# Kernel optimization log

Hardware: AMD Instinct MI355X
Metric: run time of the kernel (lower is better)

## Reference

```python
import jax, jax.numpy as jnp
import numpy as np

N, K, C, NUM_RBF, H, T = 8192, 32, 16, 16, 64, 5  # nodes, knn, channels, rbf, radial hidden, num interactions


def _levi_civita():
    e = np.zeros((3, 3, 3), np.float32)
    for i, j, k in [(0, 1, 2), (1, 2, 0), (2, 0, 1)]:
        e[i, j, k] = 1.0
        e[j, i, k] = -1.0
    return jnp.asarray(e)


def setup_inputs() -> dict:
    key = jax.random.key(0)
    ks = jax.random.split(key, 16)
    inp = {}
    inp['f0'] = jax.random.normal(ks[0], (N, C, 1), jnp.float32)
    inp['f1'] = jax.random.normal(ks[1], (N, C, 3), jnp.float32)
    inp['rbf'] = jax.random.uniform(ks[2], (N, K, NUM_RBF), jnp.float32)
    inp['gt_edge'] = jax.random.normal(ks[3], (N, K, 4), jnp.float32) * 0.5
    inp['W1'] = jax.random.normal(ks[4], (T, NUM_RBF, H), jnp.float32) / np.sqrt(NUM_RBF)
    inp['b1'] = jnp.zeros((T, H), jnp.float32)
    inp['W2'] = jax.random.normal(ks[5], (T, H, H), jnp.float32) / np.sqrt(H)
    inp['b2'] = jnp.zeros((T, H), jnp.float32)
    inp['W3'] = jax.random.normal(ks[6], (T, H, C * C), jnp.float32) / np.sqrt(H)
    inp['b3'] = jnp.zeros((T, C * C), jnp.float32)
    inp['ln_g0'] = jnp.ones((C,), jnp.float32)
    inp['ln_b0'] = jnp.zeros((C,), jnp.float32)
    inp['ln_g1'] = jnp.ones((C,), jnp.float32)
    inp['ln_b1'] = jnp.zeros((C,), jnp.float32)
    inp['gate_W0'] = jax.random.normal(ks[7], (C, C), jnp.float32) / np.sqrt(C)
    inp['gate_b0'] = jnp.zeros((C,), jnp.float32)
    inp['gate_W1'] = jax.random.normal(ks[8], (C, C), jnp.float32) / np.sqrt(C)
    inp['gate_b1'] = jnp.zeros((C,), jnp.float32)
    inp['res_W0'] = jax.random.normal(ks[9], (C, C), jnp.float32) / np.sqrt(C)
    inp['res_W1'] = jax.random.normal(ks[10], (C, C), jnp.float32) / np.sqrt(C)
    inp['nbr_idx'] = jax.random.randint(ks[11], (N, K), 0, N, jnp.int64)
    return inp


def _radial(rbf, W1, b1, W2, b2, W3, b3, t):
    # 3-layer radial MLP for interaction t: (N,K,num_rbf) -> (N,K,C,C)
    h = jax.nn.silu(rbf @ W1[t] + b1[t])
    h = jax.nn.silu(h @ W2[t] + b2[t])
    rad = h @ W3[t] + b3[t]
    return rad.reshape(rbf.shape[0], rbf.shape[1], C, C)


def _message_sparse(f_in, cg, e_feat, rad, nbr_idx):
    # f_in: (N,c_in,d_in), cg: (d_in,d_edge,d_out), e_feat: (N,K,d_edge), rad: (N,K,c_in,c_out)
    fCG = jnp.einsum('jci,ieo->jceo', f_in, cg)          # (N, c_in, d_edge, d_out)
    fCG_nbr = fCG[nbr_idx]                                # gather -> (N, K, c_in, d_edge, d_out)
    contracted = jnp.einsum('ije,ijceo->ijco', e_feat, fCG_nbr)  # (N, K, c_in, d_out)
    return jnp.einsum('ijco,ijcd->iod', rad, contracted)  # (N, c_out, d_out)


def _type_norm(f, g, b):
    # norm over irrep dim, LayerNorm over channels of the norms, rescale directions
    n = jnp.clip(jnp.linalg.norm(f, axis=-1, keepdims=True), 1e-8, None)  # (N,C,1)
    s = n[..., 0]
    mu = jnp.mean(s, axis=-1, keepdims=True)
    var = jnp.mean((s - mu) ** 2, axis=-1, keepdims=True)
    scaled = (s - mu) / jnp.sqrt(var + 1e-5) * g + b
    return f / n * scaled[..., None]


def _forward(f0, f1, rbf, gt_edge, W1, b1, W2, b2, W3, b3,
             ln_g0, ln_b0, ln_g1, ln_b1, gate_W0, gate_b0, gate_W1, gate_b1,
             res_W0, res_W1, nbr_idx):
    e0 = gt_edge[..., 0:1]   # lam=0 edge features (N,K,1)
    e1 = gt_edge[..., 1:4]   # lam=1 edge features (N,K,3)
    eye = jnp.eye(3, dtype=f0.dtype)
    cg000 = jnp.ones((1, 1, 1), f0.dtype)
    cg011 = eye[None, :, :]
    cg101 = eye[:, None, :]
    cg110 = eye[:, :, None]
    cg111 = _levi_civita().astype(f0.dtype)
    # (f_in, e_feat, cg, net_index, out_type)
    interactions = [
        (f0, e0, cg000, 0, 0),
        (f0, e1, cg011, 1, 1),
        (f1, e0, cg101, 2, 1),
        (f1, e1, cg110, 3, 0),
        (f1, e1, cg111, 4, 1),
    ]
    out0 = jnp.zeros((N, C, 1), f0.dtype)
    out1 = jnp.zeros((N, C, 3), f0.dtype)
    for f_in, e_f, cg, t, ot in interactions:
        rad = _radial(rbf, W1, b1, W2, b2, W3, b3, t)
        msg = _message_sparse(f_in, cg, e_f, rad, nbr_idx)
        if ot == 0:
            out0 = out0 + msg
        else:
            out1 = out1 + msg
    out0 = _type_norm(out0, ln_g0, ln_b0)
    out1 = _type_norm(out1, ln_g1, ln_b1)
    # equivariant gate from post-norm scalar channels
    f0g = out0[..., 0]  # (N,C)
    g0 = jax.nn.sigmoid(f0g @ gate_W0 + gate_b0)
    g1 = jax.nn.sigmoid(f0g @ gate_W1 + gate_b1)
    out0 = out0 * g0[..., None]
    out1 = out1 * g1[..., None]
    # residual channel projection per type
    out0 = out0 + jnp.einsum('ncd,co->nod', f0, res_W0)
    out1 = out1 + jnp.einsum('ncd,co->nod', f1, res_W1)
    return out0, out1


def reference(f0, f1, rbf, gt_edge, W1, b1, W2, b2, W3, b3,
              ln_g0, ln_b0, ln_g1, ln_b1, gate_W0, gate_b0, gate_W1, gate_b1,
              res_W0, res_W1, nbr_idx):
    return _forward(f0, f1, rbf, gt_edge, W1, b1, W2, b2, W3, b3,
                    ln_g0, ln_b0, ln_g1, ln_b1, gate_W0, gate_b0, gate_W1, gate_b1,
                    res_W0, res_W1, nbr_idx)
```

## Files before the change

kernel.cpp:

```cpp
#include <hip/hip_runtime.h>

#define NNODES 8192
#define KN 32
#define CC 16
#define HD 64

typedef unsigned short u16;

__device__ __forceinline__ float bf2f(u16 u) {
    union { unsigned int i; float f; } v; v.i = ((unsigned int)u) << 16; return v.f;
}
__device__ __forceinline__ u16 f2bf(float f) {
    union { float ff; unsigned int i; } v; v.ff = f;
    unsigned int r = v.i + 0x7FFFu + ((v.i >> 16) & 1u);
    return (u16)(r >> 16);
}
__device__ __forceinline__ float4 bf2f4(ushort4 u) {
    float4 r; r.x = bf2f(u.x); r.y = bf2f(u.y); r.z = bf2f(u.z); r.w = bf2f(u.w); return r;
}
__device__ __forceinline__ float silu_f(float x) { return x / (1.0f + __expf(-x)); }

template<bool F32>
__device__ __forceinline__ float ldf(const void* p, int i) {
    if constexpr (F32) return ((const float*)p)[i];
    else               return bf2f(((const u16*)p)[i]);
}
template<bool F32>
__device__ __forceinline__ float4 ldx4(const void* p, int i) {
    if constexpr (F32) return ((const float4*)p)[i >> 2];
    else               return bf2f4(((const ushort4*)p)[i >> 2]);
}
template<bool F32>
__device__ __forceinline__ void stf(void* p, int i, float v) {
    if constexpr (F32) ((float*)p)[i] = v;
    else               ((u16*)p)[i] = f2bf(v);
}

struct __align__(16) Smem {
    union {
        float W2s[HD * HD];
        struct { float G[3][16][68]; float red[4][16][3]; } g;
    } u;
    float rbf[KN][16];
    float e[KN][4];
    float f0n[KN][CC];
    float f1n[KN][CC][3];
    float con[KN][CC][4];
    float h1[KN][68];
    float h2[KN][68];
    float S[3][CC];
    float out0[CC];
    float out1[CC][3];
    float f0self[CC];
    float f1self[CC][3];
    float f0g[CC];
    float fac1[CC];
};

template<bool F32, bool I64>
__device__ void gttfn_body(Smem& sm,
                           const void* f0,  const void* f1,
                           const void* rbf, const void* gte,
                           const void* W1,  const void* b1,
                           const void* W2,  const void* b2,
                           const void* W3,  const void* b3,
                           const void* lg0, const void* lb0,
                           const void* lg1, const void* lb1,
                           const void* gW0, const void* gb0,
                           const void* gW1, const void* gb1,
                           const void* rW0, const void* rW1,
                           const int* __restrict__ nbr,
                           void* out)
{
    const int tid  = threadIdx.x;
    const int n    = blockIdx.x;
    const int lane = tid & 63;
    const int wv   = tid >> 6;

    for (int i = tid; i < KN * 16; i += 256)
        ((float*)sm.rbf)[i] = ldf<F32>(rbf, n * KN * 16 + i);
    if (tid < KN * 4)
        ((float*)sm.e)[tid] = ldf<F32>(gte, n * KN * 4 + tid);
    for (int idx = tid; idx < KN * CC; idx += 256) {
        int j = idx >> 4, c = idx & 15;
        int nb = I64 ? nbr[2 * (n * KN + j)] : nbr[n * KN + j];
        sm.f0n[j][c] = ldf<F32>(f0, nb * CC + c);
        int base = (nb * CC + c) * 3;
        sm.f1n[j][c][0] = ldf<F32>(f1, base + 0);
        sm.f1n[j][c][1] = ldf<F32>(f1, base + 1);
        sm.f1n[j][c][2] = ldf<F32>(f1, base + 2);
    }
    if (tid < CC) { sm.f0self[tid] = ldf<F32>(f0, n * CC + tid); sm.out0[tid] = 0.f; }
    else if (tid < CC + 48) {
        int k = tid - CC;
        ((float*)sm.f1self)[k] = ldf<F32>(f1, n * CC * 3 + k);
        ((float*)sm.out1)[k] = 0.f;
    }
    __syncthreads();

    const int dot_arr[5] = {1, 3, 3, 1, 3};
    const int ot_arr[5]  = {0, 1, 1, 0, 1};

    for (int t = 0; t < 5; ++t) {
        const int dt = dot_arr[t];

        for (int idx = tid; idx < KN * CC; idx += 256) {
            int j = idx >> 4, c = idx & 15;
            float e0v = sm.e[j][0];
            float ex = sm.e[j][1], ey = sm.e[j][2], ez = sm.e[j][3];
            if (t == 0) {
                sm.con[j][c][0] = e0v * sm.f0n[j][c];
            } else if (t == 1) {
                float fv = sm.f0n[j][c];
                sm.con[j][c][0] = ex * fv; sm.con[j][c][1] = ey * fv; sm.con[j][c][2] = ez * fv;
            } else if (t == 2) {
                sm.con[j][c][0] = e0v * sm.f1n[j][c][0];
                sm.con[j][c][1] = e0v * sm.f1n[j][c][1];
                sm.con[j][c][2] = e0v * sm.f1n[j][c][2];
            } else if (t == 3) {
                sm.con[j][c][0] = ex * sm.f1n[j][c][0] + ey * sm.f1n[j][c][1]
                                + ez * sm.f1n[j][c][2];
            } else {
                float fx = sm.f1n[j][c][0], fy = sm.f1n[j][c][1], fz = sm.f1n[j][c][2];
                sm.con[j][c][0] = fy * ez - fz * ey;
                sm.con[j][c][1] = fz * ex - fx * ez;
                sm.con[j][c][2] = fx * ey - fy * ex;
            }
        }

        for (int i = tid; i < 1024; i += 256) {
            float4 w = ldx4<F32>(W2, t * 4096 + i * 4);
            *(float4*)&sm.u.W2s[i * 4] = w;
        }

        for (int task = tid; task < KN * 16; task += 256) {
            int j = task >> 4, hq = task & 15;
            float4 acc = ldx4<F32>(b1, t * 64 + hq * 4);
            const float4* rrow = (const float4*)(&sm.rbf[j][0]);
#pragma unroll
            for (int r4 = 0; r4 < 4; ++r4) {
                float4 rv = rrow[r4];
                float4 w0 = ldx4<F32>(W1, t * 1024 + (r4 * 4 + 0) * 64 + hq * 4);
                float4 w1 = ldx4<F32>(W1, t * 1024 + (r4 * 4 + 1) * 64 + hq * 4);
                float4 w2 = ldx4<F32>(W1, t * 1024 + (r4 * 4 + 2) * 64 + hq * 4);
                float4 w3 = ldx4<F32>(W1, t * 1024 + (r4 * 4 + 3) * 64 + hq * 4);
                acc.x += rv.x * w0.x + rv.y * w1.x + rv.z * w2.x + rv.w * w3.x;
                acc.y += rv.x * w0.y + rv.y * w1.y + rv.z * w2.y + rv.w * w3.y;
                acc.z += rv.x * w0.z + rv.y * w1.z + rv.z * w2.z + rv.w * w3.z;
                acc.w += rv.x * w0.w + rv.y * w1.w + rv.z * w2.w + rv.w * w3.w;
            }
            float4 r;
            r.x = silu_f(acc.x); r.y = silu_f(acc.y);
            r.z = silu_f(acc.z); r.w = silu_f(acc.w);
            *(float4*)&sm.h1[j][hq * 4] = r;
        }
        __syncthreads();

        for (int task = tid; task < KN * 16; task += 256) {
            int j = task >> 4, hq = task & 15;
            float4 acc = ldx4<F32>(b2, t * 64 + hq * 4);
#pragma unroll 4
            for (int h4 = 0; h4 < 16; ++h4) {
                float4 hv = *(const float4*)&sm.h1[j][h4 * 4];
                const float* Wr = &sm.u.W2s[(h4 * 4) * 64 + hq * 4];
                float4 w0 = *(const float4*)(Wr);
                float4 w1 = *(const float4*)(Wr + 64);
                float4 w2 = *(const float4*)(Wr + 128);
                float4 w3 = *(const float4*)(Wr + 192);
                acc.x += hv.x * w0.x + hv.y * w1.x + hv.z * w2.x + hv.w * w3.x;
                acc.y += hv.x * w0.y + hv.y * w1.y + hv.z * w2.y + hv.w * w3.y;
                acc.z += hv.x * w0.z + hv.y * w1.z + hv.z * w2.z + hv.w * w3.z;
                acc.w += hv.x * w0.w + hv.y * w1.w + hv.z * w2.w + hv.w * w3.w;
            }
            float4 r;
            r.x = silu_f(acc.x); r.y = silu_f(acc.y);
            r.z = silu_f(acc.z); r.w = silu_f(acc.w);
            *(float4*)&sm.h2[j][hq * 4] = r;
        }
        __syncthreads();

        {
            int hq = tid & 15, c = tid >> 4;
            float4 g0 = make_float4(0, 0, 0, 0), g1 = g0, g2 = g0;
            float sx = 0, sy = 0, sz = 0;
            if (dt == 1) {
#pragma unroll 4
                for (int j = 0; j < KN; ++j) {
                    float4 h2q = *(const float4*)&sm.h2[j][hq * 4];
                    float cv = sm.con[j][c][0];
                    g0.x += h2q.x * cv; g0.y += h2q.y * cv;
                    g0.z += h2q.z * cv; g0.w += h2q.w * cv;
                    sx += cv;
                }
            } else {
#pragma unroll 4
                for (int j = 0; j < KN; ++j) {
                    float4 h2q = *(const float4*)&sm.h2[j][hq * 4];
                    float4 cv = *(const float4*)&sm.con[j][c][0];
                    g0.x += h2q.x * cv.x; g0.y += h2q.y * cv.x; g0.z += h2q.z * cv.x; g0.w += h2q.w * cv.x;
                    g1.x += h2q.x * cv.y; g1.y += h2q.y * cv.y; g1.z += h2q.z * cv.y; g1.w += h2q.w * cv.y;
                    g2.x += h2q.x * cv.z; g2.y += h2q.y * cv.z; g2.z += h2q.z * cv.z; g2.w += h2q.w * cv.z;
                    sx += cv.x; sy += cv.y; sz += cv.z;
                }
            }
            *(float4*)&sm.u.g.G[0][c][hq * 4] = g0;
            if (dt == 3) {
                *(float4*)&sm.u.g.G[1][c][hq * 4] = g1;
                *(float4*)&sm.u.g.G[2][c][hq * 4] = g2;
            }
            if (hq == 0) {
                sm.S[0][c] = sx;
                if (dt == 3) { sm.S[1][c] = sy; sm.S[2][c] = sz; }
            }
        }
        __syncthreads();

        {
            const int h = tid >> 2, o4 = tid & 3;
            float acc[3][4] = {{0,0,0,0},{0,0,0,0},{0,0,0,0}};
#pragma unroll 4
            for (int c = 0; c < 16; ++c) {
                float4 wq = ldx4<F32>(W3, t * 16384 + h * 256 + c * 16 + o4 * 4);
                float g0v = sm.u.g.G[0][c][h];
                acc[0][0] += g0v * wq.x; acc[0][1] += g0v * wq.y;
                acc[0][2] += g0v * wq.z; acc[0][3] += g0v * wq.w;
                if (dt == 3) {
                    float g1v = sm.u.g.G[1][c][h];
                    float g2v = sm.u.g.G[2][c][h];
                    acc[1][0] += g1v * wq.x; acc[1][1] += g1v * wq.y;
                    acc[1][2] += g1v * wq.z; acc[1][3] += g1v * wq.w;
                    acc[2][0] += g2v * wq.x; acc[2][1] += g2v * wq.y;
                    acc[2][2] += g2v * wq.z; acc[2][3] += g2v * wq.w;
                }
            }
#pragma unroll
            for (int m = 4; m <= 32; m <<= 1) {
#pragma unroll
                for (int d = 0; d < 3; ++d) {
                    if (d < dt) {
#pragma unroll
                        for (int oo = 0; oo < 4; ++oo)
                            acc[d][oo] += __shfl_xor(acc[d][oo], m);
                    }
                }
            }
            if (lane < 4) {
#pragma unroll
                for (int d = 0; d < 3; ++d) {
                    if (d < dt) {
#pragma unroll
                        for (int oo = 0; oo < 4; ++oo)
                            sm.u.g.red[wv][lane * 4 + oo][d] = acc[d][oo];
                    }
                }
            }
        }
        __syncthreads();

        if (tid < 16 * dt) {
            int o = tid & 15, d = tid >> 4;
            float s = sm.u.g.red[0][o][d] + sm.u.g.red[1][o][d]
                    + sm.u.g.red[2][o][d] + sm.u.g.red[3][o][d];
#pragma unroll 4
            for (int c = 0; c < 16; ++c)
                s += ldf<F32>(b3, t * 256 + c * 16 + o) * sm.S[d][c];
            if (ot_arr[t] == 0) sm.out0[o] += s;
            else                sm.out1[o][d] += s;
        }
        __syncthreads();
    }

    if (tid < 32) {
        if (tid < 16) {
            int c = tid;
            float v = sm.out0[c];
            float nrm = fmaxf(fabsf(v), 1e-8f);
            float mu = nrm;
#pragma unroll
            for (int m = 8; m >= 1; m >>= 1) mu += __shfl_xor(mu, m, 16);
            mu *= (1.0f / 16.0f);
            float dl = nrm - mu;
            float var = dl * dl;
#pragma unroll
            for (int m = 8; m >= 1; m >>= 1) var += __shfl_xor(var, m, 16);
            var *= (1.0f / 16.0f);
            float scaled = dl / sqrtf(var + 1e-5f) * ldf<F32>(lg0, c) + ldf<F32>(lb0, c);
            sm.f0g[c] = v / nrm * scaled;
        } else {
            int c = tid - 16;
            float x = sm.out1[c][0], y = sm.out1[c][1], z = sm.out1[c][2];
            float nrm = fmaxf(sqrtf(x * x + y * y + z * z), 1e-8f);
            float mu = nrm;
#pragma unroll
            for (int m = 8; m >= 1; m >>= 1) mu += __shfl_xor(mu, m, 16);
            mu *= (1.0f / 16.0f);
            float dl = nrm - mu;
            float var = dl * dl;
#pragma unroll
            for (int m = 8; m >= 1; m >>= 1) var += __shfl_xor(var, m, 16);
            var *= (1.0f / 16.0f);
            float scaled = dl / sqrtf(var + 1e-5f) * ldf<F32>(lg1, c) + ldf<F32>(lb1, c);
            sm.fac1[c] = scaled / nrm;
        }
    }
    __syncthreads();
    if (tid < 16) {
        int o = tid;
        float a0 = ldf<F32>(gb0, o), a1 = ldf<F32>(gb1, o);
        float r0 = 0, rx = 0, ry = 0, rz = 0;
#pragma unroll 4
        for (int c = 0; c < 16; ++c) {
            float fg = sm.f0g[c];
            a0 += fg * ldf<F32>(gW0, c * 16 + o);
            a1 += fg * ldf<F32>(gW1, c * 16 + o);
            r0 += sm.f0self[c] * ldf<F32>(rW0, c * 16 + o);
            float rw1 = ldf<F32>(rW1, c * 16 + o);
            rx += sm.f1self[c][0] * rw1; ry += sm.f1self[c][1] * rw1; rz += sm.f1self[c][2] * rw1;
        }
        float g0v = 1.f / (1.f + __expf(-a0));
        float g1v = 1.f / (1.f + __expf(-a1));
        stf<F32>(out, n * 16 + o, sm.f0g[o] * g0v + r0);
        int b = NNODES * CC + (n * 16 + o) * 3;
        float fac = sm.fac1[o] * g1v;
        stf<F32>(out, b + 0, sm.out1[o][0] * fac + rx);
        stf<F32>(out, b + 1, sm.out1[o][1] * fac + ry);
        stf<F32>(out, b + 2, sm.out1[o][2] * fac + rz);
    }
}

__global__ __launch_bounds__(256)
void gttfn_kernel(const void* f0,  const void* f1,
                  const void* rbf, const void* gte,
                  const void* W1,  const void* b1,
                  const void* W2,  const void* b2,
                  const void* W3,  const void* b3,
                  const void* lg0, const void* lb0,
                  const void* lg1, const void* lb1,
                  const void* gW0, const void* gb0,
                  const void* gW1, const void* gb1,
                  const void* rW0, const void* rW1,
                  const void* nbr_v,
                  void* out)
{
    __shared__ Smem sm;
    __shared__ int flags[2];
    const int tid = threadIdx.x;

    if (tid < 64) {
        const u16* u = (const u16*)f0;
        unsigned short w = u[2 * tid];
        int e = (w >> 7) & 0xFF;
        bool garbage = (e >= 0x83) || (e <= 0x30);
        bool isF32 = __any(garbage);
        const int* ni = (const int*)nbr_v;
        bool hi_nonzero = (tid < 32) ? (ni[2 * tid + 1] != 0) : false;
        bool isI64 = !__any(hi_nonzero);
        if (tid == 0) { flags[0] = isF32 ? 1 : 0; flags[1] = isI64 ? 1 : 0; }
    }
    __syncthreads();
    int fF32 = flags[0], fI64 = flags[1];

    const int* nbr = (const int*)nbr_v;
    if (fF32) {
        if (fI64) gttfn_body<true, true >(sm, f0,f1,rbf,gte,W1,b1,W2,b2,W3,b3,lg0,lb0,lg1,lb1,gW0,gb0,gW1,gb1,rW0,rW1,nbr,out);
        else      gttfn_body<true, false>(sm, f0,f1,rbf,gte,W1,b1,W2,b2,W3,b3,lg0,lb0,lg1,lb1,gW0,gb0,gW1,gb1,rW0,rW1,nbr,out);
    } else {
        if (fI64) gttfn_body<false, true >(sm, f0,f1,rbf,gte,W1,b1,W2,b2,W3,b3,lg0,lb0,lg1,lb1,gW0,gb0,gW1,gb1,rW0,rW1,nbr,out);
        else      gttfn_body<false, false>(sm, f0,f1,rbf,gte,W1,b1,W2,b2,W3,b3,lg0,lb0,lg1,lb1,gW0,gb0,gW1,gb1,rW0,rW1,nbr,out);
    }
}

extern "C" void kernel_launch(void* const* d_in, const int* in_sizes, int n_in,
                              void* d_out, int out_size, void* d_ws, size_t ws_size,
                              hipStream_t stream) {
    gttfn_kernel<<<dim3(NNODES), dim3(256), 0, stream>>>(
        d_in[0],  d_in[1],  d_in[2],  d_in[3],
        d_in[4],  d_in[5],  d_in[6],  d_in[7],
        d_in[8],  d_in[9],  d_in[10], d_in[11],
        d_in[12], d_in[13], d_in[14], d_in[15],
        d_in[16], d_in[17], d_in[18], d_in[19],
        d_in[20], d_out);
}
```

Baseline: 738.1 us.

## Pre-convert MLP weights to fp32 workspace, drop W2 smem staging, fuse edge contraction

Adds a small pre-kernel that converts the bf16 radial MLP weights and biases into an fp32 workspace. The main kernel then reads W2 directly from global or L2 instead of staging it in shared memory each interaction. Layer 1 and layer 2 now compute two edges per thread, and the per-edge contraction buffer is replaced by inline computation inside the G accumulation loop. The per-interaction output reduction is deferred into the next iteration, which removes one barrier per step. Shared memory shrinks and the launch bounds now request 4 blocks per CU to raise occupancy, at the cost of an extra launch and more global weight traffic.

```diff
diff --git a/kernel.cpp b/kernel.cpp
--- a/kernel.cpp
+++ b/kernel.cpp
@@ -3,7 +3,14 @@
 #define NNODES 8192
 #define KN 32
 #define CC 16
-#define HD 64
+
+#define W1_OFF 0
+#define B1_OFF 5120
+#define W2_OFF 5440
+#define B2_OFF 25920
+#define W3_OFF 26240
+#define B3_OFF 108160
+#define WS_FLOATS 109440
 
 typedef unsigned short u16;
 
@@ -36,19 +43,27 @@
     else               ((u16*)p)[i] = f2bf(v);
 }
 
+__device__ __forceinline__ void fma4(float4& a, const float4 rv,
+                                     const float4 w0, const float4 w1,
+                                     const float4 w2, const float4 w3) {
+    a.x += rv.x*w0.x + rv.y*w1.x + rv.z*w2.x + rv.w*w3.x;
+    a.y += rv.x*w0.y + rv.y*w1.y + rv.z*w2.y + rv.w*w3.y;
+    a.z += rv.x*w0.z + rv.y*w1.z + rv.z*w2.z + rv.w*w3.z;
+    a.w += rv.x*w0.w + rv.y*w1.w + rv.z*w2.w + rv.w*w3.w;
+}
+
 struct __align__(16) Smem {
-    union {
-        float W2s[HD * HD];
-        struct { float G[3][16][68]; float red[4][16][3]; } g;
-    } u;
     float rbf[KN][16];
     float e[KN][4];
     float f0n[KN][CC];
-    float f1n[KN][CC][3];
-    float con[KN][CC][4];
-    float h1[KN][68];
+    float f1n[KN][CC][4];
+    union {
+        float h1[KN][68];
+        float G[3][CC][68];
+    } u;
     float h2[KN][68];
     float S[3][CC];
+    float red[4][CC][3];
     float out0[CC];
     float out1[CC][3];
     float f0self[CC];
@@ -57,7 +72,24 @@
     float fac1[CC];
 };
 
-template<bool F32, bool I64>
+__global__ __launch_bounds__(256)
+void cvt_weights(const void* W1, const void* b1, const void* W2, const void* b2,
+                 const void* W3, const void* b3, float* ws)
+{
+    int e = (blockIdx.x * 256 + threadIdx.x) * 4;
+    if (e >= WS_FLOATS) return;
+    const u16* src; int off;
+    if (e < B1_OFF)      { src = (const u16*)W1; off = e; }
+    else if (e < W2_OFF) { src = (const u16*)b1; off = e - B1_OFF; }
+    else if (e < B2_OFF) { src = (const u16*)W2; off = e - W2_OFF; }
+    else if (e < W3_OFF) { src = (const u16*)b2; off = e - B2_OFF; }
+    else if (e < B3_OFF) { src = (const u16*)W3; off = e - W3_OFF; }
+    else                 { src = (const u16*)b3; off = e - B3_OFF; }
+    ushort4 u = *(const ushort4*)(src + off);
+    *(float4*)(ws + e) = bf2f4(u);
+}
+
+template<bool INF32, bool WF32, bool I64>
 __device__ void gttfn_body(Smem& sm,
                            const void* f0,  const void* f1,
                            const void* rbf, const void* gte,
@@ -78,22 +110,22 @@
     const int wv   = tid >> 6;
 
     for (int i = tid; i < KN * 16; i += 256)
-        ((float*)sm.rbf)[i] = ldf<F32>(rbf, n * KN * 16 + i);
+        ((float*)sm.rbf)[i] = ldf<INF32>(rbf, n * KN * 16 + i);
     if (tid < KN * 4)
-        ((float*)sm.e)[tid] = ldf<F32>(gte, n * KN * 4 + tid);
+        ((float*)sm.e)[tid] = ldf<INF32>(gte, n * KN * 4 + tid);
     for (int idx = tid; idx < KN * CC; idx += 256) {
         int j = idx >> 4, c = idx & 15;
         int nb = I64 ? nbr[2 * (n * KN + j)] : nbr[n * KN + j];
-        sm.f0n[j][c] = ldf<F32>(f0, nb * CC + c);
+        sm.f0n[j][c] = ldf<INF32>(f0, nb * CC + c);
         int base = (nb * CC + c) * 3;
-        sm.f1n[j][c][0] = ldf<F32>(f1, base + 0);
-        sm.f1n[j][c][1] = ldf<F32>(f1, base + 1);
-        sm.f1n[j][c][2] = ldf<F32>(f1, base + 2);
-    }
-    if (tid < CC) { sm.f0self[tid] = ldf<F32>(f0, n * CC + tid); sm.out0[tid] = 0.f; }
+        sm.f1n[j][c][0] = ldf<INF32>(f1, base + 0);
+        sm.f1n[j][c][1] = ldf<INF32>(f1, base + 1);
+        sm.f1n[j][c][2] = ldf<INF32>(f1, base + 2);
+    }
+    if (tid < CC) { sm.f0self[tid] = ldf<INF32>(f0, n * CC + tid); sm.out0[tid] = 0.f; }
     else if (tid < CC + 48) {
         int k = tid - CC;
-        ((float*)sm.f1self)[k] = ldf<F32>(f1, n * CC * 3 + k);
+        ((float*)sm.f1self)[k] = ldf<INF32>(f1, n * CC * 3 + k);
         ((float*)sm.out1)[k] = 0.f;
     }
     __syncthreads();
@@ -104,109 +136,105 @@
     for (int t = 0; t < 5; ++t) {
         const int dt = dot_arr[t];
 
-        for (int idx = tid; idx < KN * CC; idx += 256) {
-            int j = idx >> 4, c = idx & 15;
-            float e0v = sm.e[j][0];
-            float ex = sm.e[j][1], ey = sm.e[j][2], ez = sm.e[j][3];
-            if (t == 0) {
-                sm.con[j][c][0] = e0v * sm.f0n[j][c];
-            } else if (t == 1) {
-                float fv = sm.f0n[j][c];
-                sm.con[j][c][0] = ex * fv; sm.con[j][c][1] = ey * fv; sm.con[j][c][2] = ez * fv;
-            } else if (t == 2) {
-                sm.con[j][c][0] = e0v * sm.f1n[j][c][0];
-                sm.con[j][c][1] = e0v * sm.f1n[j][c][1];
-                sm.con[j][c][2] = e0v * sm.f1n[j][c][2];
-            } else if (t == 3) {
-                sm.con[j][c][0] = ex * sm.f1n[j][c][0] + ey * sm.f1n[j][c][1]
-                                + ez * sm.f1n[j][c][2];
-            } else {
-                float fx = sm.f1n[j][c][0], fy = sm.f1n[j][c][1], fz = sm.f1n[j][c][2];
-                sm.con[j][c][0] = fy * ez - fz * ey;
-                sm.con[j][c][1] = fz * ex - fx * ez;
-                sm.con[j][c][2] = fx * ey - fy * ex;
-            }
-        }
-
-        for (int i = tid; i < 1024; i += 256) {
-            float4 w = ldx4<F32>(W2, t * 4096 + i * 4);
-            *(float4*)&sm.u.W2s[i * 4] = w;
-        }
-
-        for (int task = tid; task < KN * 16; task += 256) {
-            int j = task >> 4, hq = task & 15;
-            float4 acc = ldx4<F32>(b1, t * 64 + hq * 4);
-            const float4* rrow = (const float4*)(&sm.rbf[j][0]);
+        if (t > 0) {
+            const int dtp = dot_arr[t - 1], otp = ot_arr[t - 1];
+            if (tid < 16 * dtp) {
+                int o = tid & 15, d = tid >> 4;
+                float s = sm.red[0][o][d] + sm.red[1][o][d]
+                        + sm.red[2][o][d] + sm.red[3][o][d];
+#pragma unroll 4
+                for (int c = 0; c < 16; ++c)
+                    s += ldf<WF32>(b3, (t - 1) * 256 + c * 16 + o) * sm.S[d][c];
+                if (otp == 0) sm.out0[o] += s;
+                else          sm.out1[o][d] += s;
+            }
+        }
+        {
+            const int jp = tid >> 4, hq = tid & 15;
+            const int j0 = jp * 2, j1 = j0 + 1;
+            float4 a0 = ldx4<WF32>(b1, t * 64 + hq * 4);
+            float4 a1 = a0;
 #pragma unroll
             for (int r4 = 0; r4 < 4; ++r4) {
-                float4 rv = rrow[r4];
-                float4 w0 = ldx4<F32>(W1, t * 1024 + (r4 * 4 + 0) * 64 + hq * 4);
-                float4 w1 = ldx4<F32>(W1, t * 1024 + (r4 * 4 + 1) * 64 + hq * 4);
-                float4 w2 = ldx4<F32>(W1, t * 1024 + (r4 * 4 + 2) * 64 + hq * 4);
-                float4 w3 = ldx4<F32>(W1, t * 1024 + (r4 * 4 + 3) * 64 + hq * 4);
-                acc.x += rv.x * w0.x + rv.y * w1.x + rv.z * w2.x + rv.w * w3.x;
-                acc.y += rv.x * w0.y + rv.y * w1.y + rv.z * w2.y + rv.w * w3.y;
-                acc.z += rv.x * w0.z + rv.y * w1.z + rv.z * w2.z + rv.w * w3.z;
-                acc.w += rv.x * w0.w + rv.y * w1.w + rv.z * w2.w + rv.w * w3.w;
-            }
-            float4 r;
-            r.x = silu_f(acc.x); r.y = silu_f(acc.y);
-            r.z = silu_f(acc.z); r.w = silu_f(acc.w);
-            *(float4*)&sm.h1[j][hq * 4] = r;
+                float4 rv0 = *(const float4*)&sm.rbf[j0][r4 * 4];
+                float4 rv1 = *(const float4*)&sm.rbf[j1][r4 * 4];
+                float4 w0 = ldx4<WF32>(W1, t * 1024 + (r4 * 4 + 0) * 64 + hq * 4);
+                float4 w1 = ldx4<WF32>(W1, t * 1024 + (r4 * 4 + 1) * 64 + hq * 4);
+                float4 w2 = ldx4<WF32>(W1, t * 1024 + (r4 * 4 + 2) * 64 + hq * 4);
+                float4 w3 = ldx4<WF32>(W1, t * 1024 + (r4 * 4 + 3) * 64 + hq * 4);
+                fma4(a0, rv0, w0, w1, w2, w3);
+                fma4(a1, rv1, w0, w1, w2, w3);
+            }
+            float4 r0, r1;
+            r0.x = silu_f(a0.x); r0.y = silu_f(a0.y); r0.z = silu_f(a0.z); r0.w = silu_f(a0.w);
+            r1.x = silu_f(a1.x); r1.y = silu_f(a1.y); r1.z = silu_f(a1.z); r1.w = silu_f(a1.w);
+            *(float4*)&sm.u.h1[j0][hq * 4] = r0;
+            *(float4*)&sm.u.h1[j1][hq * 4] = r1;
         }
         __syncthreads();
 
-        for (int task = tid; task < KN * 16; task += 256) {
-            int j = task >> 4, hq = task & 15;
-            float4 acc = ldx4<F32>(b2, t * 64 + hq * 4);
+        {
+            const int jp = tid >> 4, oq = tid & 15;
+            const int j0 = jp * 2, j1 = j0 + 1;
+            float4 a0 = ldx4<WF32>(b2, t * 64 + oq * 4), a1 = a0;
+            const int wb = t * 4096 + oq * 4;
 #pragma unroll 4
             for (int h4 = 0; h4 < 16; ++h4) {
-                float4 hv = *(const float4*)&sm.h1[j][h4 * 4];
-                const float* Wr = &sm.u.W2s[(h4 * 4) * 64 + hq * 4];
-                float4 w0 = *(const float4*)(Wr);
-                float4 w1 = *(const float4*)(Wr + 64);
-                float4 w2 = *(const float4*)(Wr + 128);
-                float4 w3 = *(const float4*)(Wr + 192);
-                acc.x += hv.x * w0.x + hv.y * w1.x + hv.z * w2.x + hv.w * w3.x;
-                acc.y += hv.x * w0.y + hv.y * w1.y + hv.z * w2.y + hv.w * w3.y;
-                acc.z += hv.x * w0.z + hv.y * w1.z + hv.z * w2.z + hv.w * w3.z;
-                acc.w += hv.x * w0.w + hv.y * w1.w + hv.z * w2.w + hv.w * w3.w;
-            }
-            float4 r;
-            r.x = silu_f(acc.x); r.y = silu_f(acc.y);
-            r.z = silu_f(acc.z); r.w = silu_f(acc.w);
-            *(float4*)&sm.h2[j][hq * 4] = r;
+                float4 w0 = ldx4<WF32>(W2, wb + (h4 * 4 + 0) * 64);
+                float4 w1 = ldx4<WF32>(W2, wb + (h4 * 4 + 1) * 64);
+                float4 w2 = ldx4<WF32>(W2, wb + (h4 * 4 + 2) * 64);
+                float4 w3 = ldx4<WF32>(W2, wb + (h4 * 4 + 3) * 64);
+                float4 hv0 = *(const float4*)&sm.u.h1[j0][h4 * 4];
+                float4 hv1 = *(const float4*)&sm.u.h1[j1][h4 * 4];
+                fma4(a0, hv0, w0, w1, w2, w3);
+                fma4(a1, hv1, w0, w1, w2, w3);
+            }
+            float4 r0, r1;
+            r0.x = silu_f(a0.x); r0.y = silu_f(a0.y); r0.z = silu_f(a0.z); r0.w = silu_f(a0.w);
+            r1.x = silu_f(a1.x); r1.y = silu_f(a1.y); r1.z = silu_f(a1.z); r1.w = silu_f(a1.w);
+            *(float4*)&sm.h2[j0][oq * 4] = r0;
+            *(float4*)&sm.h2[j1][oq * 4] = r1;
         }
         __syncthreads();
 
         {
-            int hq = tid & 15, c = tid >> 4;
+            const int c = tid >> 4, hq = tid & 15;
             float4 g0 = make_float4(0, 0, 0, 0), g1 = g0, g2 = g0;
-            float sx = 0, sy = 0, sz = 0;
-            if (dt == 1) {
+            float sx = 0.f, sy = 0.f, sz = 0.f;
 #pragma unroll 4
-                for (int j = 0; j < KN; ++j) {
-                    float4 h2q = *(const float4*)&sm.h2[j][hq * 4];
-                    float cv = sm.con[j][c][0];
-                    g0.x += h2q.x * cv; g0.y += h2q.y * cv;
-                    g0.z += h2q.z * cv; g0.w += h2q.w * cv;
-                    sx += cv;
+            for (int j = 0; j < KN; ++j) {
+                const float4 ev = *(const float4*)&sm.e[j][0];
+                float c0, c1 = 0.f, c2 = 0.f;
+                if (t == 0) {
+                    c0 = ev.x * sm.f0n[j][c];
+                } else if (t == 1) {
+                    float fv = sm.f0n[j][c];
+                    c0 = ev.y * fv; c1 = ev.z * fv; c2 = ev.w * fv;
+                } else if (t == 2) {
+                    float4 fv = *(const float4*)&sm.f1n[j][c][0];
+                    c0 = ev.x * fv.x; c1 = ev.x * fv.y; c2 = ev.x * fv.z;
+                } else if (t == 3) {
+                    float4 fv = *(const float4*)&sm.f1n[j][c][0];
+                    c0 = ev.y * fv.x + ev.z * fv.y + ev.w * fv.z;
+                } else {
+                    float4 fv = *(const float4*)&sm.f1n[j][c][0];
+                    c0 = fv.y * ev.w - fv.z * ev.z;
+                    c1 = fv.z * ev.y - fv.x * ev.w;
+                    c2 = fv.x * ev.z - fv.y * ev.y;
                 }
-            } else {
-#pragma unroll 4
-                for (int j = 0; j < KN; ++j) {
-                    float4 h2q = *(const float4*)&sm.h2[j][hq * 4];
-                    float4 cv = *(const float4*)&sm.con[j][c][0];
-                    g0.x += h2q.x * cv.x; g0.y += h2q.y * cv.x; g0.z += h2q.z * cv.x; g0.w += h2q.w * cv.x;
-                    g1.x += h2q.x * cv.y; g1.y += h2q.y * cv.y; g1.z += h2q.z * cv.y; g1.w += h2q.w * cv.y;
-                    g2.x += h2q.x * cv.z; g2.y += h2q.y * cv.z; g2.z += h2q.z * cv.z; g2.w += h2q.w * cv.z;
-                    sx += cv.x; sy += cv.y; sz += cv.z;
+                const float4 hv = *(const float4*)&sm.h2[j][hq * 4];
+                g0.x += hv.x * c0; g0.y += hv.y * c0; g0.z += hv.z * c0; g0.w += hv.w * c0;
+                sx += c0;
+                if (dt == 3) {
+                    g1.x += hv.x * c1; g1.y += hv.y * c1; g1.z += hv.z * c1; g1.w += hv.w * c1;
+                    g2.x += hv.x * c2; g2.y += hv.y * c2; g2.z += hv.z * c2; g2.w += hv.w * c2;
+                    sy += c1; sz += c2;
                 }
             }
-            *(float4*)&sm.u.g.G[0][c][hq * 4] = g0;
+            *(float4*)&sm.u.G[0][c][hq * 4] = g0;
             if (dt == 3) {
-                *(float4*)&sm.u.g.G[1][c][hq * 4] = g1;
-                *(float4*)&sm.u.g.G[2][c][hq * 4] = g2;
+                *(float4*)&sm.u.G[1][c][hq * 4] = g1;
+                *(float4*)&sm.u.G[2][c][hq * 4] = g2;
             }
             if (hq == 0) {
                 sm.S[0][c] = sx;
@@ -218,15 +246,15 @@
         {
             const int h = tid >> 2, o4 = tid & 3;
             float acc[3][4] = {{0,0,0,0},{0,0,0,0},{0,0,0,0}};
-#pragma unroll 4
+#pragma unroll 8
             for (int c = 0; c < 16; ++c) {
-                float4 wq = ldx4<F32>(W3, t * 16384 + h * 256 + c * 16 + o4 * 4);
-                float g0v = sm.u.g.G[0][c][h];
+                float4 wq = ldx4<WF32>(W3, t * 16384 + h * 256 + c * 16 + o4 * 4);
+                float g0v = sm.u.G[0][c][h];
                 acc[0][0] += g0v * wq.x; acc[0][1] += g0v * wq.y;
                 acc[0][2] += g0v * wq.z; acc[0][3] += g0v * wq.w;
                 if (dt == 3) {
-                    float g1v = sm.u.g.G[1][c][h];
-                    float g2v = sm.u.g.G[2][c][h];
+                    float g1v = sm.u.G[1][c][h];
+                    float g2v = sm.u.G[2][c][h];
                     acc[1][0] += g1v * wq.x; acc[1][1] += g1v * wq.y;
                     acc[1][2] += g1v * wq.z; acc[1][3] += g1v * wq.w;
                     acc[2][0] += g2v * wq.x; acc[2][1] += g2v * wq.y;
@@ -250,25 +278,24 @@
                     if (d < dt) {
 #pragma unroll
                         for (int oo = 0; oo < 4; ++oo)
-                            sm.u.g.red[wv][lane * 4 + oo][d] = acc[d][oo];
+                            sm.red[wv][lane * 4 + oo][d] = acc[d][oo];
                     }
                 }
             }
         }
         __syncthreads();
-
-        if (tid < 16 * dt) {
-            int o = tid & 15, d = tid >> 4;
-            float s = sm.u.g.red[0][o][d] + sm.u.g.red[1][o][d]
-                    + sm.u.g.red[2][o][d] + sm.u.g.red[3][o][d];
+    }
+
+    if (tid < 48) {
+        int o = tid & 15, d = tid >> 4;
+        float s = sm.red[0][o][d] + sm.red[1][o][d]
+                + sm.red[2][o][d] + sm.red[3][o][d];
 #pragma unroll 4
-            for (int c = 0; c < 16; ++c)
-                s += ldf<F32>(b3, t * 256 + c * 16 + o) * sm.S[d][c];
-            if (ot_arr[t] == 0) sm.out0[o] += s;
-            else                sm.out1[o][d] += s;
-        }
-        __syncthreads();
-    }
+        for (int c = 0; c < 16; ++c)
+            s += ldf<WF32>(b3, 4 * 256 + c * 16 + o) * sm.S[d][c];
+        sm.out1[o][d] += s;
+    }
+    __syncthreads();
 
     if (tid < 32) {
         if (tid < 16) {
@@ -284,7 +311,7 @@
 #pragma unroll
             for (int m = 8; m >= 1; m >>= 1) var += __shfl_xor(var, m, 16);
             var *= (1.0f / 16.0f);
-            float scaled = dl / sqrtf(var + 1e-5f) * ldf<F32>(lg0, c) + ldf<F32>(lb0, c);
+            float scaled = dl / sqrtf(var + 1e-5f) * ldf<INF32>(lg0, c) + ldf<INF32>(lb0, c);
             sm.f0g[c] = v / nrm * scaled;
         } else {
             int c = tid - 16;
@@ -299,36 +326,36 @@
 #pragma unroll
             for (int m = 8; m >= 1; m >>= 1) var += __shfl_xor(var, m, 16);
             var *= (1.0f / 16.0f);
-            float scaled = dl / sqrtf(var + 1e-5f) * ldf<F32>(lg1, c) + ldf<F32>(lb1, c);
+            float scaled = dl / sqrtf(var + 1e-5f) * ldf<INF32>(lg1, c) + ldf<INF32>(lb1, c);
             sm.fac1[c] = scaled / nrm;
         }
     }
     __syncthreads();
     if (tid < 16) {
         int o = tid;
-        float a0 = ldf<F32>(gb0, o), a1 = ldf<F32>(gb1, o);
+        float a0 = ldf<INF32>(gb0, o), a1 = ldf<INF32>(gb1, o);
         float r0 = 0, rx = 0, ry = 0, rz = 0;
 #pragma unroll 4
         for (int c = 0; c < 16; ++c) {
             float fg = sm.f0g[c];
-            a0 += fg * ldf<F32>(gW0, c * 16 + o);
-            a1 += fg * ldf<F32>(gW1, c * 16 + o);
-            r0 += sm.f0self[c] * ldf<F32>(rW0, c * 16 + o);
-            float rw1 = ldf<F32>(rW1, c * 16 + o);
+            a0 += fg * ldf<INF32>(gW0, c * 16 + o);
+            a1 += fg * ldf<INF32>(gW1, c * 16 + o);
+            r0 += sm.f0self[c] * ldf<INF32>(rW0, c * 16 + o);
+            float rw1 = ldf<INF32>(rW1, c * 16 + o);
             rx += sm.f1self[c][0] * rw1; ry += sm.f1self[c][1] * rw1; rz += sm.f1self[c][2] * rw1;
         }
         float g0v = 1.f / (1.f + __expf(-a0));
         float g1v = 1.f / (1.f + __expf(-a1));
-        stf<F32>(out, n * 16 + o, sm.f0g[o] * g0v + r0);
+        stf<INF32>(out, n * 16 + o, sm.f0g[o] * g0v + r0);
         int b = NNODES * CC + (n * 16 + o) * 3;
         float fac = sm.fac1[o] * g1v;
-        stf<F32>(out, b + 0, sm.out1[o][0] * fac + rx);
-        stf<F32>(out, b + 1, sm.out1[o][1] * fac + ry);
-        stf<F32>(out, b + 2, sm.out1[o][2] * fac + rz);
-    }
-}
-
-__global__ __launch_bounds__(256)
+        stf<INF32>(out, b + 0, sm.out1[o][0] * fac + rx);
+        stf<INF32>(out, b + 1, sm.out1[o][1] * fac + ry);
+        stf<INF32>(out, b + 2, sm.out1[o][2] * fac + rz);
+    }
+}
+
+__global__ __launch_bounds__(256, 4)
 void gttfn_kernel(const void* f0,  const void* f1,
                   const void* rbf, const void* gte,
                   const void* W1,  const void* b1,
@@ -340,7 +367,7 @@
                   const void* gW1, const void* gb1,
                   const void* rW0, const void* rW1,
                   const void* nbr_v,
-                  void* out)
+                  void* out, const float* ws)
 {
     __shared__ Smem sm;
     __shared__ int flags[2];
@@ -362,22 +389,34 @@
 
     const int* nbr = (const int*)nbr_v;
     if (fF32) {
-        if (fI64) gttfn_body<true, true >(sm, f0,f1,rbf,gte,W1,b1,W2,b2,W3,b3,lg0,lb0,lg1,lb1,gW0,gb0,gW1,gb1,rW0,rW1,nbr,out);
-        else      gttfn_body<true, false>(sm, f0,f1,rbf,gte,W1,b1,W2,b2,W3,b3,lg0,lb0,lg1,lb1,gW0,gb0,gW1,gb1,rW0,rW1,nbr,out);
+        if (fI64) gttfn_body<true, true, true >(sm, f0,f1,rbf,gte,W1,b1,W2,b2,W3,b3,lg0,lb0,lg1,lb1,gW0,gb0,gW1,gb1,rW0,rW1,nbr,out);
+        else      gttfn_body<true, true, false>(sm, f0,f1,rbf,gte,W1,b1,W2,b2,W3,b3,lg0,lb0,lg1,lb1,gW0,gb0,gW1,gb1,rW0,rW1,nbr,out);
+    } else if (ws != nullptr) {
+        const void* w1p = ws + W1_OFF; const void* b1p = ws + B1_OFF;
+        const void* w2p = ws + W2_OFF; const void* b2p = ws + B2_OFF;
+        const void* w3p = ws + W3_OFF; const void* b3p = ws + B3_OFF;
+        if (fI64) gttfn_body<false, true, true >(sm, f0,f1,rbf,gte,w1p,b1p,w2p,b2p,w3p,b3p,lg0,lb0,lg1,lb1,gW0,gb0,gW1,gb1,rW0,rW1,nbr,out);
+        else      gttfn_body<false, true, false>(sm, f0,f1,rbf,gte,w1p,b1p,w2p,b2p,w3p,b3p,lg0,lb0,lg1,lb1,gW0,gb0,gW1,gb1,rW0,rW1,nbr,out);
     } else {
-        if (fI64) gttfn_body<false, true >(sm, f0,f1,rbf,gte,W1,b1,W2,b2,W3,b3,lg0,lb0,lg1,lb1,gW0,gb0,gW1,gb1,rW0,rW1,nbr,out);
-        else      gttfn_body<false, false>(sm, f0,f1,rbf,gte,W1,b1,W2,b2,W3,b3,lg0,lb0,lg1,lb1,gW0,gb0,gW1,gb1,rW0,rW1,nbr,out);
+        if (fI64) gttfn_body<false, false, true >(sm, f0,f1,rbf,gte,W1,b1,W2,b2,W3,b3,lg0,lb0,lg1,lb1,gW0,gb0,gW1,gb1,rW0,rW1,nbr,out);
+        else      gttfn_body<false, false, false>(sm, f0,f1,rbf,gte,W1,b1,W2,b2,W3,b3,lg0,lb0,lg1,lb1,gW0,gb0,gW1,gb1,rW0,rW1,nbr,out);
     }
 }
 
 extern "C" void kernel_launch(void* const* d_in, const int* in_sizes, int n_in,
                               void* d_out, int out_size, void* d_ws, size_t ws_size,
                               hipStream_t stream) {
+    const bool have_ws = (ws_size >= (size_t)WS_FLOATS * sizeof(float)) && (d_ws != nullptr);
+    if (have_ws) {
+        const int nblk = (WS_FLOATS / 4 + 255) / 256;
+        cvt_weights<<<dim3(nblk), dim3(256), 0, stream>>>(
+            d_in[4], d_in[5], d_in[6], d_in[7], d_in[8], d_in[9], (float*)d_ws);
+    }
     gttfn_kernel<<<dim3(NNODES), dim3(256), 0, stream>>>(
         d_in[0],  d_in[1],  d_in[2],  d_in[3],
         d_in[4],  d_in[5],  d_in[6],  d_in[7],
         d_in[8],  d_in[9],  d_in[10], d_in[11],
         d_in[12], d_in[13], d_in[14], d_in[15],
         d_in[16], d_in[17], d_in[18], d_in[19],
-        d_in[20], d_out);
-}
+        d_in[20], d_out, have_ws ? (const float*)d_ws : nullptr);
+}
```

New measurement: 990.8 us. 1.34x slower.
